# Kernel optimization log

Measured on AMD Instinct MI355X. Metric: run time of the kernel, lower is better.

## Reference

```python
import jax, jax.numpy as jnp
import numpy as np

B, NOBJ, MLEN, D, H = 32, 256, 256, 1024, 16
DK = D // H
NEG = -1e9


def setup_inputs() -> dict:
    key = jax.random.key(0)
    ks = jax.random.split(key, 16)

    def lin(kw, kb, fin, fout):
        s = 1.0 / np.sqrt(fin)
        w = jax.random.uniform(kw, (fin, fout), jnp.float32, -s, s)
        b = jax.random.uniform(kb, (fout,), jnp.float32, -s, s)
        return w, b

    v = jax.random.normal(ks[0], (B, NOBJ, D), jnp.float32)
    q = jax.random.normal(ks[1], (B, MLEN, D), jnp.float32)
    v_mask = jax.random.randint(ks[2], (B, NOBJ), 0, 2).astype(jnp.float32)
    q_mask = jax.random.randint(ks[3], (B, MLEN), 0, 2).astype(jnp.float32)
    # guarantee at least one valid position per row (avoid 0/0 in masked mean)
    v_mask = v_mask.at[:, 0].set(1.0)
    q_mask = q_mask.at[:, 0].set(1.0)

    w_v4q, b_v4q = lin(ks[4], ks[5], D, D)
    w_q4v, b_q4v = lin(ks[6], ks[7], D, D)
    w_vlin, b_vlin = lin(ks[8], ks[9], D, 3 * D)
    w_qlin, b_qlin = lin(ks[10], ks[11], D, 3 * D)
    w_vout, b_vout = lin(ks[12], ks[13], D, D)
    w_qout, b_qout = lin(ks[14], ks[15], D, D)

    return dict(v=v, q=q, v_mask=v_mask, q_mask=q_mask,
                w_v4q=w_v4q, b_v4q=b_v4q, w_q4v=w_q4v, b_q4v=b_q4v,
                w_vlin=w_vlin, b_vlin=b_vlin, w_qlin=w_qlin, b_qlin=b_qlin,
                w_vout=w_vout, b_vout=b_vout, w_qout=w_qout, b_qout=b_qout)


def _attend(qh, kh, vh, mask):
    # qh,kh,vh: [B,N,D]; mask: [B,N]
    b, n, _ = qh.shape
    qh = qh.reshape(b, n, H, DK)
    kh = kh.reshape(b, n, H, DK)
    vh = vh.reshape(b, n, H, DK)
    scores = jnp.einsum('bqhd,bkhd->bhqk', qh, kh)
    # faithful to torch: masked_fill(-1e9) THEN divide by sqrt(dk)
    scores = jnp.where(mask[:, None, None, :] == 0, NEG, scores) / np.sqrt(DK)
    attn = jax.nn.softmax(scores, axis=-1)
    out = jnp.einsum('bhqk,bkhd->bqhd', attn, vh)
    return out.reshape(b, n, H * DK)


def reference(v, q, v_mask, q_mask,
              w_v4q, b_v4q, w_q4v, b_q4v,
              w_vlin, b_vlin, w_qlin, b_qlin,
              w_vout, b_vout, w_qout, b_qout):
    v_mean = (v * v_mask[:, :, None]).sum(1) / v_mask.sum(1, keepdims=True)
    q_mean = (q * q_mask[:, :, None]).sum(1) / q_mask.sum(1, keepdims=True)
    v4q_gate = jax.nn.sigmoid(jax.nn.relu(v_mean) @ w_v4q + b_v4q)[:, None, :]
    q4v_gate = jax.nn.sigmoid(jax.nn.relu(q_mean) @ w_q4v + b_q4v)[:, None, :]

    v_trans = (jax.nn.relu(v) @ w_vlin + b_vlin) * v_mask[:, :, None]
    q_trans = (jax.nn.relu(q) @ w_qlin + b_qlin) * q_mask[:, :, None]
    v_k, v_q, v_v = jnp.split(v_trans, 3, axis=2)
    q_k, q_q, q_v = jnp.split(q_trans, 3, axis=2)

    v_update = _attend((1 + q4v_gate) * v_q, (1 + q4v_gate) * v_k, v_v, v_mask)
    q_update = _attend((1 + v4q_gate) * q_q, (1 + v4q_gate) * q_k, q_v, q_mask)

    updated_v = (v + v_update) @ w_vout + b_vout
    updated_q = (q + q_update) @ w_qout + b_qout
    return updated_v, updated_q
```

## Files before the change

### kernel.cpp

```cpp
#include <hip/hip_runtime.h>
#include <cstdint>

typedef unsigned short u16;
typedef __attribute__((ext_vector_type(8))) short s16x8;
typedef __attribute__((ext_vector_type(4))) float f32x4;

__device__ __forceinline__ u16 f2bf(float f) {
  unsigned int u = __float_as_uint(f);
  return (u16)((u + 0x7FFFu + ((u >> 16) & 1u)) >> 16);
}
__device__ __forceinline__ float bf2f(u16 b) {
  return __uint_as_float(((unsigned int)b) << 16);
}
__device__ __forceinline__ f32x4 mfma16(s16x8 a, s16x8 b, f32x4 c) {
  return __builtin_amdgcn_mfma_f32_16x16x32_bf16(a, b, c, 0, 0, 0);
}
__device__ __forceinline__ void gload16(const void* g, void* l) {
  __builtin_amdgcn_global_load_lds((const __attribute__((address_space(1))) void*)g,
                                   (__attribute__((address_space(3))) void*)l, 16, 0, 0);
}

__global__ __launch_bounds__(256) void k_wt(const float* __restrict__ in0, u16* __restrict__ out0,
                                            const float* __restrict__ in1, u16* __restrict__ out1,
                                            int K, int N) {
  const float* in = blockIdx.z ? in1 : in0;
  u16* out = blockIdx.z ? out1 : out0;
  __shared__ float tile[32][33];
  int n0 = blockIdx.x * 32, k0 = blockIdx.y * 32;
  int tx = threadIdx.x & 31, ty = threadIdx.x >> 5;
#pragma unroll
  for (int i = 0; i < 32; i += 8)
    tile[ty + i][tx] = in[(size_t)(k0 + ty + i) * N + n0 + tx];
  __syncthreads();
#pragma unroll
  for (int i = 0; i < 32; i += 8)
    out[(size_t)(n0 + ty + i) * K + k0 + tx] = f2bf(tile[tx][ty + i]);
}

__global__ __launch_bounds__(256) void k_prep(const float* __restrict__ v,
                                              const float* __restrict__ q,
                                              const float* __restrict__ vm,
                                              const float* __restrict__ qm,
                                              u16* __restrict__ rbf,
                                              float* __restrict__ raw,
                                              float* __restrict__ msum) {
  int b = blockIdx.x;
  int mod = blockIdx.y & 1, dc = blockIdx.y >> 1;
  int ns = blockIdx.z;
  const float* x = mod ? q : v;
  const float* mk = (mod ? qm : vm) + b * 256;
  int d = dc * 256 + threadIdx.x;
  const float* xb = x + ((size_t)b * 256 + ns * 32) * 1024 + d;
  u16* ob = rbf + ((size_t)(mod * 8192 + b * 256 + ns * 32)) * 1024 + d;
  float s = 0.f;
#pragma unroll 4
  for (int n = 0; n < 32; ++n) {
    float xv = xb[(size_t)n * 1024];
    s = fmaf(xv, mk[ns * 32 + n], s);
    ob[(size_t)n * 1024] = f2bf(xv > 0.f ? xv : 0.f);
  }
  atomicAdd(&raw[(mod * 32 + b) * 1024 + d], s);
  if (threadIdx.x == 0 && dc == 0) {
    float t = 0.f;
    for (int n = 0; n < 32; ++n) t += mk[ns * 32 + n];
    atomicAdd(&msum[mod * 32 + b], t);
  }
}

__global__ __launch_bounds__(256) void k_gate(const float* __restrict__ raw,
                                              const float* __restrict__ msum,
                                              const float* __restrict__ Wq4v,
                                              const float* __restrict__ bq4v,
                                              const float* __restrict__ Wv4q,
                                              const float* __restrict__ bv4q,
                                              float* __restrict__ gsv,
                                              float* __restrict__ gsq) {
  int b = blockIdx.y, z = blockIdx.z;
  int srcmod = z == 0 ? 1 : 0;
  const float* W = z == 0 ? Wq4v : Wv4q;
  const float* bias = z == 0 ? bq4v : bv4q;
  float* gs = z == 0 ? gsv : gsq;
  const float* r = raw + (srcmod * 32 + b) * 1024;
  float inv = 1.f / msum[srcmod * 32 + b];
  int d = blockIdx.x * 256 + threadIdx.x;
  float acc = bias[d];
#pragma unroll 8
  for (int k = 0; k < 1024; ++k) {
    float m = r[k] * inv;
    m = m > 0.f ? m : 0.f;
    acc = fmaf(m, W[(size_t)k * 1024 + d], acc);
  }
  gs[b * 1024 + d] = 1.f + 1.f / (1.f + expf(-acc));
}

template <int EPI>
__global__ __launch_bounds__(512, 2) void k_mm(const u16* __restrict__ A,
                                               const u16* __restrict__ BTv,
                                               const u16* __restrict__ BTq,
                                               const float* __restrict__ biasv,
                                               const float* __restrict__ biasq,
                                               u16* __restrict__ outv_b,
                                               u16* __restrict__ outq_b,
                                               float* __restrict__ outf,
                                               const float* __restrict__ maskv,
                                               const float* __restrict__ maskq,
                                               const float* __restrict__ gsv,
                                               const float* __restrict__ gsq) {
  __shared__ u16 lA[4][8192];
  __shared__ u16 lB[4][8192];
  int nwg = gridDim.x, cpx = nwg >> 3, bid = blockIdx.x;
  int id = (bid & 7) * cpx + (bid >> 3);
  int by = id & 63, bx = id >> 6;
  int m0 = by * 256, n0 = bx * 256;
  int half = (m0 >= 8192);
  const u16* BT = half ? BTq : BTv;

  int tid = threadIdx.x, w = tid >> 6, lane = tid & 63;
  int wr = w >> 2, wc = w & 3;
  int la = lane & 15, lb = lane >> 4;

  int o0 = tid * 16, o1 = 8192 + tid * 16;
  int r0 = o0 >> 6, c0 = o0 & 63;
  int r1 = o1 >> 6, c1 = o1 & 63;
  const char* sA0 = (const char*)A + (size_t)(m0 + r0) * 2048 + (c0 ^ (((r0 >> 1) & 3) << 4));
  const char* sA1 = (const char*)A + (size_t)(m0 + r1) * 2048 + (c1 ^ (((r1 >> 1) & 3) << 4));
  const char* sB0 = (const char*)BT + (size_t)(n0 + r0) * 2048 + (c0 ^ (((r0 >> 1) & 3) << 4));
  const char* sB1 = (const char*)BT + (size_t)(n0 + r1) * 2048 + (c1 ^ (((r1 >> 1) & 3) << 4));

  auto stA = [&](int slot, int kt, int kh) {
    int go = kt * 128 + kh * 64;
    gload16(sA0 + go, (char*)&lA[slot][0] + o0);
    gload16(sA1 + go, (char*)&lA[slot][0] + o1);
  };
  auto stB = [&](int slot, int kt, int kh) {
    int go = kt * 128 + kh * 64;
    gload16(sB0 + go, (char*)&lB[slot][0] + o0);
    gload16(sB1 + go, (char*)&lB[slot][0] + o1);
  };

  int aoffs[8], boffs[4];
#pragma unroll
  for (int i = 0; i < 8; ++i) {
    int r = wr * 128 + i * 16 + la;
    aoffs[i] = r * 64 + ((lb * 16) ^ (((r >> 1) & 3) << 4));
  }
#pragma unroll
  for (int j = 0; j < 4; ++j) {
    int r = wc * 64 + j * 16 + la;
    boffs[j] = r * 64 + ((lb * 16) ^ (((r >> 1) & 3) << 4));
  }

  f32x4 acc[8][4] = {};
  s16x8 a[8], b[2];

  auto rdA8 = [&](int slot) {
#pragma unroll
    for (int i = 0; i < 8; ++i)
      a[i] = *(const s16x8*)((const char*)&lA[slot][0] + aoffs[i]);
  };
  auto rdB2 = [&](int slot, int jh) {
    b[0] = *(const s16x8*)((const char*)&lB[slot][0] + boffs[jh * 2]);
    b[1] = *(const s16x8*)((const char*)&lB[slot][0] + boffs[jh * 2 + 1]);
  };
  auto gate = [&]() {
    __builtin_amdgcn_s_barrier();
    asm volatile("s_waitcnt lgkmcnt(0)" ::: "memory");
    __builtin_amdgcn_sched_barrier(0);
    __builtin_amdgcn_s_setprio(1);
  };
  auto mfJ0 = [&]() {
#pragma unroll
    for (int i = 0; i < 8; ++i) {
      acc[i][0] = mfma16(a[i], b[0], acc[i][0]);
      acc[i][1] = mfma16(a[i], b[1], acc[i][1]);
    }
  };
  auto mfJ1 = [&]() {
#pragma unroll
    for (int i = 0; i < 8; ++i) {
      acc[i][2] = mfma16(a[i], b[0], acc[i][2]);
      acc[i][3] = mfma16(a[i], b[1], acc[i][3]);
    }
  };
  auto close = [&]() {
    __builtin_amdgcn_s_setprio(0);
    __builtin_amdgcn_s_barrier();
  };

  stA(0, 0, 0); stB(0, 0, 0); stA(1, 0, 1); stB(1, 0, 1);
  stA(2, 1, 0); stB(2, 1, 0); stA(3, 1, 1);
  asm volatile("s_waitcnt vmcnt(6)" ::: "memory");
  __builtin_amdgcn_s_barrier();

#pragma unroll 1
  for (int it = 0; it < 8; ++it) {
    int k1t = 2 * it + 1, nx = 2 * it + 2, nx2 = 2 * it + 3;
    bool pf = it < 7;
    rdA8(0); rdB2(0, 0);
    stB(3, k1t, 1);
    gate(); mfJ0(); close();
    rdB2(0, 1);
    if (pf) stA(0, nx, 0);
    gate(); mfJ1(); close();
    rdA8(1); rdB2(1, 0);
    if (pf) stB(0, nx, 0);
    gate(); mfJ0(); close();
    rdB2(1, 1);
    if (pf) stA(1, nx, 1);
    gate(); mfJ1();
    __builtin_amdgcn_s_setprio(0);
    if (pf) asm volatile("s_waitcnt vmcnt(6)" ::: "memory");
    else    asm volatile("s_waitcnt vmcnt(0)" ::: "memory");
    __builtin_amdgcn_s_barrier();
    rdA8(2); rdB2(2, 0);
    if (pf) stB(1, nx, 1);
    gate(); mfJ0(); close();
    rdB2(2, 1);
    if (pf) stA(2, nx2, 0);
    gate(); mfJ1(); close();
    rdA8(3); rdB2(3, 0);
    if (pf) stB(2, nx2, 0);
    gate(); mfJ0(); close();
    rdB2(3, 1);
    if (pf) stA(3, nx2, 1);
    gate(); mfJ1();
    __builtin_amdgcn_s_setprio(0);
    if (pf) asm volatile("s_waitcnt vmcnt(6)" ::: "memory");
    else    asm volatile("s_waitcnt vmcnt(0)" ::: "memory");
    __builtin_amdgcn_s_barrier();
  }

  const float* bias = half ? biasq : biasv;
  const float* mask = half ? maskq : maskv;
  const float* gs = half ? gsq : gsv;
#pragma unroll
  for (int i = 0; i < 8; ++i) {
    int mbase = m0 + wr * 128 + i * 16 + lb * 4;
#pragma unroll
    for (int j = 0; j < 4; ++j) {
      int n = n0 + wc * 64 + j * 16 + la;
      float bn = bias[n];
#pragma unroll
      for (int r = 0; r < 4; ++r) {
        int m = mbase + r;
        float val = acc[i][j][r] + bn;
        if (EPI == 0) {
          int mloc = m & 8191;
          val *= mask[mloc];
          if (n < 2048) val *= gs[((mloc >> 8) << 10) + (n & 1023)];
          (half ? outq_b : outv_b)[(size_t)mloc * 3072 + n] = f2bf(val);
        } else {
          outf[(size_t)m * 1024 + n] = val;
        }
      }
    }
  }
}

__global__ __launch_bounds__(256) void k_vtrans(const u16* __restrict__ tr0,
                                                const u16* __restrict__ tr1,
                                                u16* __restrict__ vt0,
                                                u16* __restrict__ vt1) {
  int bz = blockIdx.z;
  int mod = bz >> 5, b = bz & 31;
  const u16* tr = mod ? tr1 : tr0;
  u16* vt = mod ? vt1 : vt0;
  __shared__ u16 tile[64 * 64];
  int kt = blockIdx.x, dt = blockIdx.y;
  int t = threadIdx.x, tx = t & 7, ty = t >> 3;
  const u16* src = tr + (size_t)b * 786432 + 2048 + dt * 64;
#pragma unroll
  for (int i = 0; i < 2; ++i) {
    int key = ty + i * 32;
    s16x8 vv = *(const s16x8*)(src + (size_t)(kt * 64 + key) * 3072 + tx * 8);
    int oct = key >> 3;
#pragma unroll
    for (int j = 0; j < 8; ++j) {
      int d = tx * 8 + j;
      tile[d * 64 + ((oct ^ (d >> 3)) << 3) + (key & 7)] = (u16)vv[j];
    }
  }
  __syncthreads();
  u16* dst = vt + (size_t)b * 262144 + (size_t)dt * 64 * 256 + kt * 64;
#pragma unroll
  for (int i = 0; i < 2; ++i) {
    int d = ty + i * 32;
    s16x8 ov = *(const s16x8*)&tile[d * 64 + ((tx ^ (d >> 3)) << 3)];
    *(s16x8*)(dst + (size_t)d * 256 + tx * 8) = ov;
  }
}

__global__ __launch_bounds__(256) void k_attn(const u16* __restrict__ tr0,
                                              const u16* __restrict__ tr1,
                                              const u16* __restrict__ vt0,
                                              const u16* __restrict__ vt1,
                                              const float* __restrict__ mk0,
                                              const float* __restrict__ mk1,
                                              const float* __restrict__ x0,
                                              const float* __restrict__ x1,
                                              u16* __restrict__ ao0,
                                              u16* __restrict__ ao1) {
  int z = blockIdx.z;
  const u16* trans = z ? tr1 : tr0;
  const u16* vt = z ? vt1 : vt0;
  const float* mask = z ? mk1 : mk0;
  const float* xorig = z ? x1 : x0;
  u16* attin = z ? ao1 : ao0;

  __shared__ u16 Kl[16384];
  __shared__ u16 Vt[64 * 256];
  int h = blockIdx.x >> 2, qc = blockIdx.x & 3;
  int b = blockIdx.y;
  int t = threadIdx.x, w = t >> 6, lane = t & 63;
  const u16* tb = trans + (size_t)b * 256 * 3072;
  const char* tbc = (const char*)tb;

#pragma unroll
  for (int i = 0; i < 8; ++i) {
    int o = i * 4096 + t * 16;
    int row = o >> 7, colb = o & 127;
    gload16(tbc + (size_t)row * 6144 + h * 128 + (colb ^ ((row & 7) << 4)),
            (char*)Kl + o);
  }
  const char* vtb = (const char*)(vt + (size_t)b * 262144 + (size_t)h * 64 * 256);
#pragma unroll
  for (int i = 0; i < 8; ++i) {
    int o = i * 4096 + t * 16;
    int d = o >> 9, oct = (o >> 4) & 31;
    gload16(vtb + d * 512 + ((oct ^ (d & 7)) << 4), (char*)Vt + o);
  }
  __syncthreads();

  int la = lane & 15, lb = lane >> 4;
  int q0 = qc * 64 + w * 16;
  const u16* qrow = tb + (size_t)(q0 + la) * 3072 + 1024 + h * 64;
  s16x8 qf0 = *(const s16x8*)(qrow + lb * 8);
  s16x8 qf1 = *(const s16x8*)(qrow + 32 + lb * 8);

  f32x4 sc[16];
#pragma unroll
  for (int nt = 0; nt < 16; ++nt) {
    int row = nt * 16 + la;
    int sw = (row & 7) << 4;
    s16x8 kf0 = *(const s16x8*)((const char*)Kl + row * 128 + ((lb * 16) ^ sw));
    s16x8 kf1 = *(const s16x8*)((const char*)Kl + row * 128 + ((64 + lb * 16) ^ sw));
    f32x4 s = {0.f, 0.f, 0.f, 0.f};
    s = mfma16(qf0, kf0, s);
    s = mfma16(qf1, kf1, s);
    sc[nt] = s;
  }
  __syncthreads();

  u16* Pw = Kl + w * 4096;
  const float* mb = mask + b * 256;
  float rsum[4] = {0.f, 0.f, 0.f, 0.f};
#pragma unroll
  for (int nt = 0; nt < 16; ++nt) {
    int key = nt * 16 + la;
    float km = mb[key];
    int quad = key >> 3, klow = key & 7;
#pragma unroll
    for (int r = 0; r < 4; ++r) {
      float p = (km != 0.f) ? expf(sc[nt][r] * 0.125f) : 0.f;
      u16 pb = f2bf(p);
      int lr = lb * 4 + r;
      rsum[r] += bf2f(pb);
      Pw[lr * 256 + ((quad ^ (lr & 7)) << 3) + klow] = pb;
    }
  }
#pragma unroll
  for (int r = 0; r < 4; ++r) {
    rsum[r] += __shfl_xor(rsum[r], 1);
    rsum[r] += __shfl_xor(rsum[r], 2);
    rsum[r] += __shfl_xor(rsum[r], 4);
    rsum[r] += __shfl_xor(rsum[r], 8);
  }
  __syncthreads();

  f32x4 o[4] = {};
  for (int kt = 0; kt < 8; ++kt) {
    int pq = kt * 4 + lb;
    s16x8 pa = *(const s16x8*)&Pw[la * 256 + ((pq ^ (la & 7)) << 3)];
#pragma unroll
    for (int dt = 0; dt < 4; ++dt) {
      int d = dt * 16 + la;
      s16x8 vb = *(const s16x8*)&Vt[d * 256 + ((pq ^ (d & 7)) << 3)];
      o[dt] = mfma16(pa, vb, o[dt]);
    }
  }

#pragma unroll
  for (int dt = 0; dt < 4; ++dt) {
    int dcol = h * 64 + dt * 16 + la;
#pragma unroll
    for (int r = 0; r < 4; ++r) {
      int qr = q0 + lb * 4 + r;
      size_t gi = ((size_t)b * 256 + qr) * 1024 + dcol;
      attin[gi] = f2bf(xorig[gi] + o[dt][r] / rsum[r]);
    }
  }
}

extern "C" void kernel_launch(void* const* d_in, const int* in_sizes, int n_in,
                              void* d_out, int out_size, void* d_ws, size_t ws_size,
                              hipStream_t stream) {
  const float* v      = (const float*)d_in[0];
  const float* q      = (const float*)d_in[1];
  const float* v_mask = (const float*)d_in[2];
  const float* q_mask = (const float*)d_in[3];
  const float* w_v4q  = (const float*)d_in[4];
  const float* b_v4q  = (const float*)d_in[5];
  const float* w_q4v  = (const float*)d_in[6];
  const float* b_q4v  = (const float*)d_in[7];
  const float* w_vlin = (const float*)d_in[8];
  const float* b_vlin = (const float*)d_in[9];
  const float* w_qlin = (const float*)d_in[10];
  const float* b_qlin = (const float*)d_in[11];
  const float* w_vout = (const float*)d_in[12];
  const float* b_vout = (const float*)d_in[13];
  const float* w_qout = (const float*)d_in[14];
  const float* b_qout = (const float*)d_in[15];
  float* out = (float*)d_out;

  char* ws = (char*)d_ws;
  u16* rbf       = (u16*)(ws);
  u16* rbf_v     = rbf;
  u16* rbf_q     = (u16*)(ws + 16777216);
  u16* woutT_v   = (u16*)(ws + 33554432);
  u16* woutT_q   = (u16*)(ws + 35651584);
  u16* trans_v   = (u16*)(ws + 37748736);
  u16* wlinT_v   = (u16*)(ws + 88080384);
  u16* wlinT_q   = (u16*)(ws + 94371840);
  float* raw     = (float*)(ws + 100663296);
  float* msum    = (float*)(ws + 100925440);
  float* gs_v    = (float*)(ws + 100925696);
  float* gs_q    = (float*)(ws + 101056768);
  u16* vT_v      = (u16*)(ws + 88080384);
  u16* trans_q   = (u16*)d_out;
  u16* vT_q      = (u16*)((char*)d_out + 50331648);

  dim3 blk(256);
  hipMemsetAsync(raw, 0, 262400, stream);
  k_wt<<<dim3(96, 32, 2), blk, 0, stream>>>(w_vlin, wlinT_v, w_qlin, wlinT_q, 1024, 3072);
  k_wt<<<dim3(32, 32, 2), blk, 0, stream>>>(w_vout, woutT_v, w_qout, woutT_q, 1024, 1024);
  k_prep<<<dim3(32, 8, 8), blk, 0, stream>>>(v, q, v_mask, q_mask, rbf, raw, msum);
  k_gate<<<dim3(4, 32, 2), blk, 0, stream>>>(raw, msum, w_q4v, b_q4v, w_v4q, b_v4q, gs_v, gs_q);
  k_mm<0><<<dim3(768), dim3(512), 0, stream>>>(rbf, wlinT_v, wlinT_q, b_vlin, b_qlin,
                                               trans_v, trans_q, nullptr,
                                               v_mask, q_mask, gs_v, gs_q);
  k_vtrans<<<dim3(4, 16, 64), blk, 0, stream>>>(trans_v, trans_q, vT_v, vT_q);
  k_attn<<<dim3(64, 32, 2), blk, 0, stream>>>(trans_v, trans_q, vT_v, vT_q,
                                              v_mask, q_mask, v, q, rbf_v, rbf_q);
  k_mm<1><<<dim3(256), dim3(512), 0, stream>>>(rbf, woutT_v, woutT_q, b_vout, b_qout,
                                               nullptr, nullptr, out,
                                               nullptr, nullptr, nullptr, nullptr);
}
```

Before: 536.8 us.

## Fuse V transpose into attention kernel and loop query chunks per block

Removes the separate k_vtrans kernel: each attention block now loads V directly from the projection output and transposes it into LDS itself. The grid shrinks from 64 to 16 blocks per (batch, modality), and each block loops over the four query chunks, so K and V are loaded once per head rather than once per chunk. A separate P buffer is added in LDS, which raises shared-memory use and may lower occupancy, and parallelism per launch drops fourfold. The k_mm block-to-tile mapping is also changed to group tiles per XCD differently for cache locality.

```diff
diff --git a/kernel.cpp b/kernel.cpp
--- a/kernel.cpp
+++ b/kernel.cpp
@@ -108,9 +108,10 @@
                                                const float* __restrict__ gsq) {
   __shared__ u16 lA[4][8192];
   __shared__ u16 lB[4][8192];
-  int nwg = gridDim.x, cpx = nwg >> 3, bid = blockIdx.x;
-  int id = (bid & 7) * cpx + (bid >> 3);
-  int by = id & 63, bx = id >> 6;
+  int bid = blockIdx.x;
+  int xcd = bid & 7, local = bid >> 3;
+  int by = xcd * 8 + (local & 7);
+  int bx = local >> 3;
   int m0 = by * 256, n0 = bx * 256;
   int half = (m0 >= 8192);
   const u16* BT = half ? BTq : BTv;
@@ -257,43 +258,8 @@
   }
 }
 
-__global__ __launch_bounds__(256) void k_vtrans(const u16* __restrict__ tr0,
-                                                const u16* __restrict__ tr1,
-                                                u16* __restrict__ vt0,
-                                                u16* __restrict__ vt1) {
-  int bz = blockIdx.z;
-  int mod = bz >> 5, b = bz & 31;
-  const u16* tr = mod ? tr1 : tr0;
-  u16* vt = mod ? vt1 : vt0;
-  __shared__ u16 tile[64 * 64];
-  int kt = blockIdx.x, dt = blockIdx.y;
-  int t = threadIdx.x, tx = t & 7, ty = t >> 3;
-  const u16* src = tr + (size_t)b * 786432 + 2048 + dt * 64;
-#pragma unroll
-  for (int i = 0; i < 2; ++i) {
-    int key = ty + i * 32;
-    s16x8 vv = *(const s16x8*)(src + (size_t)(kt * 64 + key) * 3072 + tx * 8);
-    int oct = key >> 3;
-#pragma unroll
-    for (int j = 0; j < 8; ++j) {
-      int d = tx * 8 + j;
-      tile[d * 64 + ((oct ^ (d >> 3)) << 3) + (key & 7)] = (u16)vv[j];
-    }
-  }
-  __syncthreads();
-  u16* dst = vt + (size_t)b * 262144 + (size_t)dt * 64 * 256 + kt * 64;
-#pragma unroll
-  for (int i = 0; i < 2; ++i) {
-    int d = ty + i * 32;
-    s16x8 ov = *(const s16x8*)&tile[d * 64 + ((tx ^ (d >> 3)) << 3)];
-    *(s16x8*)(dst + (size_t)d * 256 + tx * 8) = ov;
-  }
-}
-
 __global__ __launch_bounds__(256) void k_attn(const u16* __restrict__ tr0,
                                               const u16* __restrict__ tr1,
-                                              const u16* __restrict__ vt0,
-                                              const u16* __restrict__ vt1,
                                               const float* __restrict__ mk0,
                                               const float* __restrict__ mk1,
                                               const float* __restrict__ x0,
@@ -302,17 +268,16 @@
                                               u16* __restrict__ ao1) {
   int z = blockIdx.z;
   const u16* trans = z ? tr1 : tr0;
-  const u16* vt = z ? vt1 : vt0;
   const float* mask = z ? mk1 : mk0;
   const float* xorig = z ? x1 : x0;
   u16* attin = z ? ao1 : ao0;
 
   __shared__ u16 Kl[16384];
-  __shared__ u16 Vt[64 * 256];
-  int h = blockIdx.x >> 2, qc = blockIdx.x & 3;
-  int b = blockIdx.y;
+  __shared__ u16 Vt[16384];
+  __shared__ u16 P[16384];
+  int h = blockIdx.x, b = blockIdx.y;
   int t = threadIdx.x, w = t >> 6, lane = t & 63;
-  const u16* tb = trans + (size_t)b * 256 * 3072;
+  const u16* tb = trans + (size_t)b * 786432;
   const char* tbc = (const char*)tb;
 
 #pragma unroll
@@ -322,82 +287,91 @@
     gload16(tbc + (size_t)row * 6144 + h * 128 + (colb ^ ((row & 7) << 4)),
             (char*)Kl + o);
   }
-  const char* vtb = (const char*)(vt + (size_t)b * 262144 + (size_t)h * 64 * 256);
 #pragma unroll
   for (int i = 0; i < 8; ++i) {
-    int o = i * 4096 + t * 16;
-    int d = o >> 9, oct = (o >> 4) & 31;
-    gload16(vtb + d * 512 + ((oct ^ (d & 7)) << 4), (char*)Vt + o);
+    int c = t + i * 256;
+    int key = c >> 3, dc = c & 7;
+    s16x8 vv = *(const s16x8*)(tb + (size_t)key * 3072 + 2048 + h * 64 + dc * 8);
+    int quad = key >> 3, klow = key & 7;
+#pragma unroll
+    for (int j = 0; j < 8; ++j) {
+      int d = dc * 8 + j;
+      Vt[d * 256 + ((quad ^ (d & 7)) << 3) + klow] = (u16)vv[j];
+    }
   }
   __syncthreads();
 
   int la = lane & 15, lb = lane >> 4;
-  int q0 = qc * 64 + w * 16;
-  const u16* qrow = tb + (size_t)(q0 + la) * 3072 + 1024 + h * 64;
-  s16x8 qf0 = *(const s16x8*)(qrow + lb * 8);
-  s16x8 qf1 = *(const s16x8*)(qrow + 32 + lb * 8);
-
-  f32x4 sc[16];
-#pragma unroll
-  for (int nt = 0; nt < 16; ++nt) {
-    int row = nt * 16 + la;
-    int sw = (row & 7) << 4;
-    s16x8 kf0 = *(const s16x8*)((const char*)Kl + row * 128 + ((lb * 16) ^ sw));
-    s16x8 kf1 = *(const s16x8*)((const char*)Kl + row * 128 + ((64 + lb * 16) ^ sw));
-    f32x4 s = {0.f, 0.f, 0.f, 0.f};
-    s = mfma16(qf0, kf0, s);
-    s = mfma16(qf1, kf1, s);
-    sc[nt] = s;
-  }
-  __syncthreads();
-
-  u16* Pw = Kl + w * 4096;
   const float* mb = mask + b * 256;
-  float rsum[4] = {0.f, 0.f, 0.f, 0.f};
-#pragma unroll
-  for (int nt = 0; nt < 16; ++nt) {
-    int key = nt * 16 + la;
-    float km = mb[key];
-    int quad = key >> 3, klow = key & 7;
+  u16* Pw = P + w * 4096;
+
+#pragma unroll 1
+  for (int qc = 0; qc < 4; ++qc) {
+    int q0 = qc * 64 + w * 16;
+    const u16* qrow = tb + (size_t)(q0 + la) * 3072 + 1024 + h * 64;
+    s16x8 qf0 = *(const s16x8*)(qrow + lb * 8);
+    s16x8 qf1 = *(const s16x8*)(qrow + 32 + lb * 8);
+
+    f32x4 sc[16];
+#pragma unroll
+    for (int nt = 0; nt < 16; ++nt) {
+      int row = nt * 16 + la;
+      int sw = (row & 7) << 4;
+      s16x8 kf0 = *(const s16x8*)((const char*)Kl + row * 128 + ((lb * 16) ^ sw));
+      s16x8 kf1 = *(const s16x8*)((const char*)Kl + row * 128 + ((64 + lb * 16) ^ sw));
+      f32x4 s = {0.f, 0.f, 0.f, 0.f};
+      s = mfma16(qf0, kf0, s);
+      s = mfma16(qf1, kf1, s);
+      sc[nt] = s;
+    }
+
+    float rsum[4] = {0.f, 0.f, 0.f, 0.f};
+#pragma unroll
+    for (int nt = 0; nt < 16; ++nt) {
+      int key = nt * 16 + la;
+      float km = mb[key];
+      int quad = key >> 3, klow = key & 7;
+#pragma unroll
+      for (int r = 0; r < 4; ++r) {
+        float p = (km != 0.f) ? expf(sc[nt][r] * 0.125f) : 0.f;
+        u16 pb = f2bf(p);
+        int lr = lb * 4 + r;
+        rsum[r] += bf2f(pb);
+        Pw[lr * 256 + ((quad ^ (lr & 7)) << 3) + klow] = pb;
+      }
+    }
 #pragma unroll
     for (int r = 0; r < 4; ++r) {
-      float p = (km != 0.f) ? expf(sc[nt][r] * 0.125f) : 0.f;
-      u16 pb = f2bf(p);
-      int lr = lb * 4 + r;
-      rsum[r] += bf2f(pb);
-      Pw[lr * 256 + ((quad ^ (lr & 7)) << 3) + klow] = pb;
-    }
-  }
-#pragma unroll
-  for (int r = 0; r < 4; ++r) {
-    rsum[r] += __shfl_xor(rsum[r], 1);
-    rsum[r] += __shfl_xor(rsum[r], 2);
-    rsum[r] += __shfl_xor(rsum[r], 4);
-    rsum[r] += __shfl_xor(rsum[r], 8);
-  }
-  __syncthreads();
-
-  f32x4 o[4] = {};
-  for (int kt = 0; kt < 8; ++kt) {
-    int pq = kt * 4 + lb;
-    s16x8 pa = *(const s16x8*)&Pw[la * 256 + ((pq ^ (la & 7)) << 3)];
+      rsum[r] += __shfl_xor(rsum[r], 1);
+      rsum[r] += __shfl_xor(rsum[r], 2);
+      rsum[r] += __shfl_xor(rsum[r], 4);
+      rsum[r] += __shfl_xor(rsum[r], 8);
+    }
+    __syncthreads();
+
+    f32x4 o[4] = {};
+    for (int kt = 0; kt < 8; ++kt) {
+      int pq = kt * 4 + lb;
+      s16x8 pa = *(const s16x8*)&Pw[la * 256 + ((pq ^ (la & 7)) << 3)];
+#pragma unroll
+      for (int dt = 0; dt < 4; ++dt) {
+        int d = dt * 16 + la;
+        s16x8 vb = *(const s16x8*)&Vt[d * 256 + ((pq ^ (d & 7)) << 3)];
+        o[dt] = mfma16(pa, vb, o[dt]);
+      }
+    }
+
 #pragma unroll
     for (int dt = 0; dt < 4; ++dt) {
-      int d = dt * 16 + la;
-      s16x8 vb = *(const s16x8*)&Vt[d * 256 + ((pq ^ (d & 7)) << 3)];
-      o[dt] = mfma16(pa, vb, o[dt]);
-    }
-  }
-
-#pragma unroll
-  for (int dt = 0; dt < 4; ++dt) {
-    int dcol = h * 64 + dt * 16 + la;
-#pragma unroll
-    for (int r = 0; r < 4; ++r) {
-      int qr = q0 + lb * 4 + r;
-      size_t gi = ((size_t)b * 256 + qr) * 1024 + dcol;
-      attin[gi] = f2bf(xorig[gi] + o[dt][r] / rsum[r]);
-    }
+      int dcol = h * 64 + dt * 16 + la;
+#pragma unroll
+      for (int r = 0; r < 4; ++r) {
+        int qr = q0 + lb * 4 + r;
+        size_t gi = ((size_t)b * 256 + qr) * 1024 + dcol;
+        attin[gi] = f2bf(xorig[gi] + o[dt][r] / rsum[r]);
+      }
+    }
+    __syncthreads();
   }
 }
 
@@ -435,9 +409,7 @@
   float* msum    = (float*)(ws + 100925440);
   float* gs_v    = (float*)(ws + 100925696);
   float* gs_q    = (float*)(ws + 101056768);
-  u16* vT_v      = (u16*)(ws + 88080384);
   u16* trans_q   = (u16*)d_out;
-  u16* vT_q      = (u16*)((char*)d_out + 50331648);
 
   dim3 blk(256);
   hipMemsetAsync(raw, 0, 262400, stream);
@@ -448,8 +420,7 @@
   k_mm<0><<<dim3(768), dim3(512), 0, stream>>>(rbf, wlinT_v, wlinT_q, b_vlin, b_qlin,
                                                trans_v, trans_q, nullptr,
                                                v_mask, q_mask, gs_v, gs_q);
-  k_vtrans<<<dim3(4, 16, 64), blk, 0, stream>>>(trans_v, trans_q, vT_v, vT_q);
-  k_attn<<<dim3(64, 32, 2), blk, 0, stream>>>(trans_v, trans_q, vT_v, vT_q,
+  k_attn<<<dim3(16, 32, 2), blk, 0, stream>>>(trans_v, trans_q,
                                               v_mask, q_mask, v, q, rbf_v, rbf_q);
   k_mm<1><<<dim3(256), dim3(512), 0, stream>>>(rbf, woutT_v, woutT_q, b_vout, b_qout,
                                                nullptr, nullptr, out,
```

Result: slower. 570.5 us (+6.3%).
